# Kernel tuning notes

Measured on AMD Instinct MI355X. Metric: run time of the kernel, lower is better.

Reference implementation:

```python
import jax, jax.numpy as jnp
import numpy as np

N_NODES = 100000
N_EDGES = 1600000
D = 128
NEG_SLOPE = 0.01  # torch F.leaky_relu default


def setup_inputs() -> dict:
    key = jax.random.key(0)
    k1, k2, k3, k4, k5, k6 = jax.random.split(key, 6)
    input = jax.random.normal(k1, (N_NODES, D), dtype=jnp.float32)
    edge_row = jax.random.randint(k2, (N_EDGES,), 0, N_NODES, dtype=jnp.int32)
    edge_col = jax.random.randint(k3, (N_EDGES,), 0, N_NODES, dtype=jnp.int32)
    edge_val = jax.random.uniform(k4, (N_EDGES,), dtype=jnp.float32)
    # learned params: W1: Linear(D, D, bias=False), W2: Linear(2D, D, bias=False)
    # torch stores weight as [out, in]; apply as x @ W.T
    bound1 = 1.0 / np.sqrt(D)
    bound2 = 1.0 / np.sqrt(2 * D)
    W1 = jax.random.uniform(k5, (D, D), dtype=jnp.float32, minval=-bound1, maxval=bound1)
    W2 = jax.random.uniform(k6, (D, 2 * D), dtype=jnp.float32, minval=-bound2, maxval=bound2)
    return {"input": input, "edge_row": edge_row, "edge_col": edge_col,
            "edge_val": edge_val, "W1": W1, "W2": W2}


def reference(input, edge_row, edge_col, edge_val, W1, W2):
    # proj_input = W1(input)
    proj = input @ W1.T                                   # [N, D]
    # neighboor = spmm(adj, proj): out[i] = sum_e val[e] * proj[col[e]] for row[e]==i
    msg = edge_val[:, None] * proj[edge_col]              # [E, D]
    neigh = jax.ops.segment_sum(msg, edge_row, num_segments=input.shape[0])  # [N, D]
    h = jnp.concatenate([input + neigh, input * neigh], axis=-1)  # [N, 2D]
    return jax.nn.leaky_relu(h @ W2.T, NEG_SLOPE)         # [N, D]
```

## Files before the change

### kernel.cpp

```cpp
#include <hip/hip_runtime.h>

#define DIM 128
#define BROWS 128
#define BCAP 3072
#define NBUK_PAD 800
#define BK_EDGES 6144

typedef __attribute__((ext_vector_type(8))) short short8;
typedef __attribute__((ext_vector_type(4))) float f32x4;

__device__ __forceinline__ unsigned short f2bf(float f) {
    unsigned u = __float_as_uint(f);
    u += 0x7fffu + ((u >> 16) & 1u);
    return (unsigned short)(u >> 16);
}
__device__ __forceinline__ float bf2f(unsigned short b) {
    return __uint_as_float(((unsigned)b) << 16);
}

__global__ void k_zero(int* __restrict__ gcur, int nbuk) {
    int i = threadIdx.x;
    if (i < nbuk) gcur[i] = 0;
}

__global__ __launch_bounds__(1024) void k_prep(const float4* __restrict__ in,
                                               const float* __restrict__ W1,
                                               const float* __restrict__ W2,
                                               const int* __restrict__ er,
                                               const int* __restrict__ ec,
                                               const float* __restrict__ ev,
                                               int* __restrict__ gcur,
                                               int2* __restrict__ edata0,
                                               unsigned short* __restrict__ inputb,
                                               unsigned short* __restrict__ w1b,
                                               unsigned short* __restrict__ w2b,
                                               int E, int nbuk, int nBkt, int n4) {
    __shared__ int2 sed[BK_EDGES];
    __shared__ int lhist[NBUK_PAD];
    __shared__ int lscan[NBUK_PAD];
    __shared__ int lpos[NBUK_PAD];
    __shared__ int gbase[NBUK_PAD];
    int b = blockIdx.x, tid = threadIdx.x;

    if (b < nBkt) {
        if (tid < NBUK_PAD) lhist[tid] = 0;
        __syncthreads();
        int e0 = b * BK_EDGES;
        int bcnt = E - e0; if (bcnt > BK_EDGES) bcnt = BK_EDGES;
        for (int i = tid; i < bcnt; i += 1024)
            atomicAdd(&lhist[er[e0 + i] >> 7], 1);
        __syncthreads();
        if (tid < NBUK_PAD) lscan[tid] = lhist[tid];
        __syncthreads();
        for (int off = 1; off < NBUK_PAD; off <<= 1) {
            int v = (tid < NBUK_PAD && tid >= off) ? lscan[tid - off] : 0;
            __syncthreads();
            if (tid < NBUK_PAD) lscan[tid] += v;
            __syncthreads();
        }
        if (tid < NBUK_PAD) {
            int c = lhist[tid];
            lpos[tid] = lscan[tid] - c;
            gbase[tid] = (c > 0 && tid < nbuk) ? atomicAdd(&gcur[tid], c) : 0;
        }
        __syncthreads();
        for (int i = tid; i < bcnt; i += 1024) {
            int e = e0 + i;
            int r = er[e], bk = r >> 7;
            int p = atomicAdd(&lpos[bk], 1);
            sed[p] = make_int2(((r & 127) << 17) | ec[e], __float_as_int(ev[e]));
        }
        __syncthreads();
        int sub = tid & 7, bg = tid >> 3;
        for (int bk = bg; bk < nbuk; bk += 128) {
            int c = lhist[bk];
            if (c == 0) continue;
            int excl = lscan[bk] - c;
            int gb = gbase[bk];
            long base = (long)bk * BCAP;
            for (int j = sub; j < c; j += 8)
                if (gb + j < BCAP)
                    edata0[base + gb + j] = sed[excl + j];
        }
    } else if (b < nBkt + 48) {
        int idx = (b - nBkt) * 1024 + tid;
        if (idx < 16384)      w1b[idx] = f2bf(W1[idx]);
        else                  w2b[idx - 16384] = f2bf(W2[idx - 16384]);
    } else {
        int i = (b - nBkt - 48) * 1024 + tid;
        if (i < n4) {
            float4 v = in[i];
            *(ushort4*)(inputb + (long)i * 4) =
                make_ushort4(f2bf(v.x), f2bf(v.y), f2bf(v.z), f2bf(v.w));
        }
    }
}

__global__ __launch_bounds__(512) void k_gather(const unsigned short* __restrict__ xb,
                                                const int2* __restrict__ edata0,
                                                const int* __restrict__ gcur,
                                                unsigned short* __restrict__ aggb, int N) {
    __shared__ int2 sed[BCAP];
    __shared__ int hist[BROWS];
    __shared__ int hscan[BROWS];
    __shared__ int lcur[BROWS];
    int tid = threadIdx.x, b = blockIdx.x;
    int cnt = gcur[b]; if (cnt > BCAP) cnt = BCAP;
    const int2* e0 = edata0 + (long)b * BCAP;
    if (tid < BROWS) hist[tid] = 0;
    __syncthreads();
    for (int i = tid; i < cnt; i += 512) atomicAdd(&hist[e0[i].x >> 17], 1);
    __syncthreads();
    if (tid < BROWS) hscan[tid] = hist[tid];
    __syncthreads();
    for (int off = 1; off < BROWS; off <<= 1) {
        int v = (tid < BROWS && tid >= off) ? hscan[tid - off] : 0;
        __syncthreads();
        if (tid < BROWS) hscan[tid] += v;
        __syncthreads();
    }
    if (tid < BROWS) lcur[tid] = hscan[tid] - hist[tid];
    __syncthreads();
    for (int i = tid; i < cnt; i += 512) {
        int2 v = e0[i];
        int p = atomicAdd(&lcur[v.x >> 17], 1);
        sed[p] = make_int2(v.x & 0x1FFFF, v.y);
    }
    __syncthreads();

    int slot = tid >> 4, s = tid & 15;
    const int4* x4 = (const int4*)xb;

#define ACC8(U, V)                                                         \
    {                                                                      \
        const unsigned* wp_ = (const unsigned*)&(U);                       \
        pa[0] += (V) * __uint_as_float(wp_[0] << 16);                      \
        pa[1] += (V) * __uint_as_float(wp_[0] & 0xffff0000u);              \
        pa[2] += (V) * __uint_as_float(wp_[1] << 16);                      \
        pa[3] += (V) * __uint_as_float(wp_[1] & 0xffff0000u);              \
        pa[4] += (V) * __uint_as_float(wp_[2] << 16);                      \
        pa[5] += (V) * __uint_as_float(wp_[2] & 0xffff0000u);              \
        pa[6] += (V) * __uint_as_float(wp_[3] << 16);                      \
        pa[7] += (V) * __uint_as_float(wp_[3] & 0xffff0000u);              \
    }

    for (int k = 0; k < 4; ++k) {
        int rl = k * 32 + slot;
        int row = b * BROWS + rl;
        int beg = hscan[rl] - hist[rl], end = hscan[rl];
        float pa[8];
#pragma unroll
        for (int t = 0; t < 8; ++t) pa[t] = 0.f;
        int j = beg;
        for (; j + 4 <= end; j += 4) {
            int2 q0 = sed[j], q1 = sed[j + 1], q2 = sed[j + 2], q3 = sed[j + 3];
            int4 u0 = x4[(long)q0.x * 16 + s];
            int4 u1 = x4[(long)q1.x * 16 + s];
            int4 u2 = x4[(long)q2.x * 16 + s];
            int4 u3 = x4[(long)q3.x * 16 + s];
            float v0 = __int_as_float(q0.y), v1 = __int_as_float(q1.y);
            float v2 = __int_as_float(q2.y), v3 = __int_as_float(q3.y);
            ACC8(u0, v0);
            ACC8(u1, v1);
            ACC8(u2, v2);
            ACC8(u3, v3);
        }
        for (; j < end; ++j) {
            int2 q = sed[j];
            int4 u = x4[(long)q.x * 16 + s];
            float v = __int_as_float(q.y);
            ACC8(u, v);
        }
        if (row < N) {
            short8 o;
#pragma unroll
            for (int t = 0; t < 8; ++t) o[t] = (short)f2bf(pa[t]);
            *(short8*)(aggb + (long)row * DIM + s * 8) = o;
        }
    }
#undef ACC8
}

__global__ __launch_bounds__(256, 3) void k_fused(const unsigned short* __restrict__ aggb,
                                                  const unsigned short* __restrict__ inputb,
                                                  const unsigned short* __restrict__ w1b,
                                                  const unsigned short* __restrict__ w2b,
                                                  float* __restrict__ out, int N) {
    __shared__ __align__(16) unsigned short sh[2 * 64 * 136];
    __shared__ __align__(16) unsigned short xs[64 * 136];
    int w = threadIdx.x >> 6, lane = threadIdx.x & 63;
    int quad = lane >> 4, lq = lane & 15;
    int blk0 = blockIdx.x * 64;
    unsigned short* sh0 = sh;
    unsigned short* sh1 = sh + 64 * 136;

    for (int i = threadIdx.x; i < 64 * 16; i += 256) {
        int row = i >> 4, c = i & 15;
        int rr = blk0 + row; if (rr >= N) rr = N - 1;
        *(short8*)(xs + row * 136 + c * 8) =
            *(const short8*)(inputb + (long)rr * DIM + c * 8);
    }

    short8 b1[2][4];
#pragma unroll
    for (int ntl = 0; ntl < 2; ++ntl)
#pragma unroll
        for (int kb = 0; kb < 4; ++kb)
            b1[ntl][kb] = *(const short8*)(w1b + ((w * 2 + ntl) * 16 + lq) * DIM +
                                           kb * 32 + quad * 8);
    __syncthreads();

#pragma unroll
    for (int mt = 0; mt < 4; ++mt) {
        short8 afr[4];
        {
            int row = blk0 + mt * 16 + lq; if (row >= N) row = N - 1;
#pragma unroll
            for (int kb = 0; kb < 4; ++kb)
                afr[kb] = *(const short8*)(aggb + (long)row * DIM + kb * 32 + quad * 8);
        }
#pragma unroll
        for (int ntl = 0; ntl < 2; ++ntl) {
            f32x4 c = {0.f, 0.f, 0.f, 0.f};
#pragma unroll
            for (int kb = 0; kb < 4; ++kb)
                c = __builtin_amdgcn_mfma_f32_16x16x32_bf16(afr[kb], b1[ntl][kb], c, 0, 0, 0);
            int nt = w * 2 + ntl;
#pragma unroll
            for (int rg = 0; rg < 4; ++rg) {
                int lrow = mt * 16 + quad * 4 + rg;
                float x = bf2f(xs[lrow * 136 + nt * 16 + lq]);
                float nb = c[rg];
                int off = lrow * 136 + nt * 16 + lq;
                sh0[off] = f2bf(x + nb);
                sh1[off] = f2bf(x * nb);
            }
        }
    }

    short8 b2[2][8];
#pragma unroll
    for (int ntl = 0; ntl < 2; ++ntl)
#pragma unroll
        for (int kb = 0; kb < 8; ++kb)
            b2[ntl][kb] = *(const short8*)(w2b + ((w * 2 + ntl) * 16 + lq) * 256 +
                                           kb * 32 + quad * 8);
    __syncthreads();

#pragma unroll
    for (int mt = 0; mt < 4; ++mt) {
        int arow = (mt * 16 + lq) * 136;
        short8 a0[4], a1[4];
#pragma unroll
        for (int kb = 0; kb < 4; ++kb) {
            a0[kb] = *(const short8*)(sh0 + arow + kb * 32 + quad * 8);
            a1[kb] = *(const short8*)(sh1 + arow + kb * 32 + quad * 8);
        }
#pragma unroll
        for (int ntl = 0; ntl < 2; ++ntl) {
            f32x4 c = {0.f, 0.f, 0.f, 0.f};
#pragma unroll
            for (int kb = 0; kb < 4; ++kb)
                c = __builtin_amdgcn_mfma_f32_16x16x32_bf16(a0[kb], b2[ntl][kb], c, 0, 0, 0);
#pragma unroll
            for (int kb = 0; kb < 4; ++kb)
                c = __builtin_amdgcn_mfma_f32_16x16x32_bf16(a1[kb], b2[ntl][kb + 4], c, 0, 0, 0);
            int nt = w * 2 + ntl;
#pragma unroll
            for (int rg = 0; rg < 4; ++rg) {
                int r = blk0 + mt * 16 + quad * 4 + rg;
                if (r < N) {
                    float v = c[rg];
                    v = (v > 0.f) ? v : 0.01f * v;
                    out[(long)r * DIM + nt * 16 + lq] = v;
                }
            }
        }
    }
}

extern "C" void kernel_launch(void* const* d_in, const int* in_sizes, int n_in,
                              void* d_out, int out_size, void* d_ws, size_t ws_size,
                              hipStream_t stream) {
    const float* input = (const float*)d_in[0];
    const int*   er    = (const int*)d_in[1];
    const int*   ec    = (const int*)d_in[2];
    const float* ev    = (const float*)d_in[3];
    const float* W1    = (const float*)d_in[4];
    const float* W2    = (const float*)d_in[5];
    int N = in_sizes[0] / DIM;
    int E = in_sizes[1];
    float* out = (float*)d_out;
    int nbuk = (N + BROWS - 1) / BROWS;

    int* ws = (int*)d_ws;
    int* gcur = ws;
    int2* edata0 = (int2*)(ws + 1024);
    unsigned short* w1b = (unsigned short*)(edata0 + (long)nbuk * BCAP);
    unsigned short* w2b = w1b + 16384;
    unsigned short* inputb = w2b + 32768;
    unsigned short* aggb = inputb + (long)N * DIM;

    int n4 = N * (DIM / 4);
    int nBkt = (E + BK_EDGES - 1) / BK_EDGES;
    int nCvt = (n4 + 1023) / 1024;

    k_zero<<<1, 1024, 0, stream>>>(gcur, nbuk);

    k_prep<<<nBkt + 48 + nCvt, 1024, 0, stream>>>(
        (const float4*)input, W1, W2, er, ec, ev, gcur, edata0,
        inputb, w1b, w2b, E, nbuk, nBkt, n4);

    k_gather<<<nbuk, 512, 0, stream>>>(inputb, edata0, gcur, aggb, N);

    k_fused<<<(N + 63) / 64, 256, 0, stream>>>(aggb, inputb, w1b, w2b, out, N);
}
```

Before: 233.9 us.

## Halve fused GEMM shared tiles, unroll gather by 8, memset counters

The fused GEMM kernel now processes its 64 rows in two 32-row halves. This halves shared memory per block, loads W2 fragments per column tile instead of holding them all in registers, and raises the occupancy hint from 3 to 4 blocks. The gather inner loop gains an 8-edge unrolled stage so more independent global loads are in flight. The zeroing kernel is replaced by hipMemsetAsync. The trade-offs are an extra sync per half and W2 fragments being reloaded for each half.

```diff
diff --git a/kernel.cpp b/kernel.cpp
--- a/kernel.cpp
+++ b/kernel.cpp
@@ -16,11 +16,6 @@
 }
 __device__ __forceinline__ float bf2f(unsigned short b) {
     return __uint_as_float(((unsigned)b) << 16);
-}
-
-__global__ void k_zero(int* __restrict__ gcur, int nbuk) {
-    int i = threadIdx.x;
-    if (i < nbuk) gcur[i] = 0;
 }
 
 __global__ __launch_bounds__(1024) void k_prep(const float4* __restrict__ in,
@@ -152,24 +147,41 @@
 #pragma unroll
         for (int t = 0; t < 8; ++t) pa[t] = 0.f;
         int j = beg;
+        for (; j + 8 <= end; j += 8) {
+            int2 q0 = sed[j],     q1 = sed[j + 1], q2 = sed[j + 2], q3 = sed[j + 3];
+            int2 q4 = sed[j + 4], q5 = sed[j + 5], q6 = sed[j + 6], q7 = sed[j + 7];
+            int4 u0 = x4[(long)q0.x * 16 + s];
+            int4 u1 = x4[(long)q1.x * 16 + s];
+            int4 u2 = x4[(long)q2.x * 16 + s];
+            int4 u3 = x4[(long)q3.x * 16 + s];
+            int4 u4 = x4[(long)q4.x * 16 + s];
+            int4 u5 = x4[(long)q5.x * 16 + s];
+            int4 u6 = x4[(long)q6.x * 16 + s];
+            int4 u7 = x4[(long)q7.x * 16 + s];
+            ACC8(u0, __int_as_float(q0.y));
+            ACC8(u1, __int_as_float(q1.y));
+            ACC8(u2, __int_as_float(q2.y));
+            ACC8(u3, __int_as_float(q3.y));
+            ACC8(u4, __int_as_float(q4.y));
+            ACC8(u5, __int_as_float(q5.y));
+            ACC8(u6, __int_as_float(q6.y));
+            ACC8(u7, __int_as_float(q7.y));
+        }
         for (; j + 4 <= end; j += 4) {
             int2 q0 = sed[j], q1 = sed[j + 1], q2 = sed[j + 2], q3 = sed[j + 3];
             int4 u0 = x4[(long)q0.x * 16 + s];
             int4 u1 = x4[(long)q1.x * 16 + s];
             int4 u2 = x4[(long)q2.x * 16 + s];
             int4 u3 = x4[(long)q3.x * 16 + s];
-            float v0 = __int_as_float(q0.y), v1 = __int_as_float(q1.y);
-            float v2 = __int_as_float(q2.y), v3 = __int_as_float(q3.y);
-            ACC8(u0, v0);
-            ACC8(u1, v1);
-            ACC8(u2, v2);
-            ACC8(u3, v3);
+            ACC8(u0, __int_as_float(q0.y));
+            ACC8(u1, __int_as_float(q1.y));
+            ACC8(u2, __int_as_float(q2.y));
+            ACC8(u3, __int_as_float(q3.y));
         }
         for (; j < end; ++j) {
             int2 q = sed[j];
             int4 u = x4[(long)q.x * 16 + s];
-            float v = __int_as_float(q.y);
-            ACC8(u, v);
+            ACC8(u, __int_as_float(q.y));
         }
         if (row < N) {
             short8 o;
@@ -181,25 +193,18 @@
 #undef ACC8
 }
 
-__global__ __launch_bounds__(256, 3) void k_fused(const unsigned short* __restrict__ aggb,
+__global__ __launch_bounds__(256, 4) void k_fused(const unsigned short* __restrict__ aggb,
                                                   const unsigned short* __restrict__ inputb,
                                                   const unsigned short* __restrict__ w1b,
                                                   const unsigned short* __restrict__ w2b,
                                                   float* __restrict__ out, int N) {
-    __shared__ __align__(16) unsigned short sh[2 * 64 * 136];
-    __shared__ __align__(16) unsigned short xs[64 * 136];
+    __shared__ __align__(16) unsigned short sh[2 * 32 * 136];
+    __shared__ __align__(16) unsigned short xs[32 * 136];
     int w = threadIdx.x >> 6, lane = threadIdx.x & 63;
     int quad = lane >> 4, lq = lane & 15;
     int blk0 = blockIdx.x * 64;
     unsigned short* sh0 = sh;
-    unsigned short* sh1 = sh + 64 * 136;
-
-    for (int i = threadIdx.x; i < 64 * 16; i += 256) {
-        int row = i >> 4, c = i & 15;
-        int rr = blk0 + row; if (rr >= N) rr = N - 1;
-        *(short8*)(xs + row * 136 + c * 8) =
-            *(const short8*)(inputb + (long)rr * DIM + c * 8);
-    }
+    unsigned short* sh1 = sh + 32 * 136;
 
     short8 b1[2][4];
 #pragma unroll
@@ -208,71 +213,77 @@
         for (int kb = 0; kb < 4; ++kb)
             b1[ntl][kb] = *(const short8*)(w1b + ((w * 2 + ntl) * 16 + lq) * DIM +
                                            kb * 32 + quad * 8);
-    __syncthreads();
-
-#pragma unroll
-    for (int mt = 0; mt < 4; ++mt) {
-        short8 afr[4];
-        {
-            int row = blk0 + mt * 16 + lq; if (row >= N) row = N - 1;
-#pragma unroll
-            for (int kb = 0; kb < 4; ++kb)
-                afr[kb] = *(const short8*)(aggb + (long)row * DIM + kb * 32 + quad * 8);
-        }
+
+    for (int half = 0; half < 2; ++half) {
+        int base = blk0 + half * 32;
+
+        for (int i = threadIdx.x; i < 32 * 16; i += 256) {
+            int row = i >> 4, c = i & 15;
+            int rr = base + row; if (rr >= N) rr = N - 1;
+            *(short8*)(xs + row * 136 + c * 8) =
+                *(const short8*)(inputb + (long)rr * DIM + c * 8);
+        }
+        __syncthreads();
+
+#pragma unroll
+        for (int mt = 0; mt < 2; ++mt) {
+            short8 afr[4];
+            {
+                int row = base + mt * 16 + lq; if (row >= N) row = N - 1;
+#pragma unroll
+                for (int kb = 0; kb < 4; ++kb)
+                    afr[kb] = *(const short8*)(aggb + (long)row * DIM + kb * 32 + quad * 8);
+            }
+#pragma unroll
+            for (int ntl = 0; ntl < 2; ++ntl) {
+                f32x4 c = {0.f, 0.f, 0.f, 0.f};
+#pragma unroll
+                for (int kb = 0; kb < 4; ++kb)
+                    c = __builtin_amdgcn_mfma_f32_16x16x32_bf16(afr[kb], b1[ntl][kb], c, 0, 0, 0);
+                int nt = w * 2 + ntl;
+#pragma unroll
+                for (int rg = 0; rg < 4; ++rg) {
+                    int lrow = mt * 16 + quad * 4 + rg;
+                    float x = bf2f(xs[lrow * 136 + nt * 16 + lq]);
+                    float nb = c[rg];
+                    int off = lrow * 136 + nt * 16 + lq;
+                    sh0[off] = f2bf(x + nb);
+                    sh1[off] = f2bf(x * nb);
+                }
+            }
+        }
+        __syncthreads();
+
 #pragma unroll
         for (int ntl = 0; ntl < 2; ++ntl) {
-            f32x4 c = {0.f, 0.f, 0.f, 0.f};
-#pragma unroll
-            for (int kb = 0; kb < 4; ++kb)
-                c = __builtin_amdgcn_mfma_f32_16x16x32_bf16(afr[kb], b1[ntl][kb], c, 0, 0, 0);
+            short8 bb[8];
+#pragma unroll
+            for (int kb = 0; kb < 8; ++kb)
+                bb[kb] = *(const short8*)(w2b + ((w * 2 + ntl) * 16 + lq) * 256 +
+                                          kb * 32 + quad * 8);
             int nt = w * 2 + ntl;
 #pragma unroll
-            for (int rg = 0; rg < 4; ++rg) {
-                int lrow = mt * 16 + quad * 4 + rg;
-                float x = bf2f(xs[lrow * 136 + nt * 16 + lq]);
-                float nb = c[rg];
-                int off = lrow * 136 + nt * 16 + lq;
-                sh0[off] = f2bf(x + nb);
-                sh1[off] = f2bf(x * nb);
-            }
-        }
-    }
-
-    short8 b2[2][8];
-#pragma unroll
-    for (int ntl = 0; ntl < 2; ++ntl)
-#pragma unroll
-        for (int kb = 0; kb < 8; ++kb)
-            b2[ntl][kb] = *(const short8*)(w2b + ((w * 2 + ntl) * 16 + lq) * 256 +
-                                           kb * 32 + quad * 8);
-    __syncthreads();
-
-#pragma unroll
-    for (int mt = 0; mt < 4; ++mt) {
-        int arow = (mt * 16 + lq) * 136;
-        short8 a0[4], a1[4];
-#pragma unroll
-        for (int kb = 0; kb < 4; ++kb) {
-            a0[kb] = *(const short8*)(sh0 + arow + kb * 32 + quad * 8);
-            a1[kb] = *(const short8*)(sh1 + arow + kb * 32 + quad * 8);
-        }
-#pragma unroll
-        for (int ntl = 0; ntl < 2; ++ntl) {
-            f32x4 c = {0.f, 0.f, 0.f, 0.f};
-#pragma unroll
-            for (int kb = 0; kb < 4; ++kb)
-                c = __builtin_amdgcn_mfma_f32_16x16x32_bf16(a0[kb], b2[ntl][kb], c, 0, 0, 0);
-#pragma unroll
-            for (int kb = 0; kb < 4; ++kb)
-                c = __builtin_amdgcn_mfma_f32_16x16x32_bf16(a1[kb], b2[ntl][kb + 4], c, 0, 0, 0);
-            int nt = w * 2 + ntl;
-#pragma unroll
-            for (int rg = 0; rg < 4; ++rg) {
-                int r = blk0 + mt * 16 + quad * 4 + rg;
-                if (r < N) {
-                    float v = c[rg];
-                    v = (v > 0.f) ? v : 0.01f * v;
-                    out[(long)r * DIM + nt * 16 + lq] = v;
+            for (int mt = 0; mt < 2; ++mt) {
+                int arow = (mt * 16 + lq) * 136;
+                f32x4 c = {0.f, 0.f, 0.f, 0.f};
+#pragma unroll
+                for (int kb = 0; kb < 4; ++kb) {
+                    short8 a0 = *(const short8*)(sh0 + arow + kb * 32 + quad * 8);
+                    c = __builtin_amdgcn_mfma_f32_16x16x32_bf16(a0, bb[kb], c, 0, 0, 0);
+                }
+#pragma unroll
+                for (int kb = 0; kb < 4; ++kb) {
+                    short8 a1 = *(const short8*)(sh1 + arow + kb * 32 + quad * 8);
+                    c = __builtin_amdgcn_mfma_f32_16x16x32_bf16(a1, bb[kb + 4], c, 0, 0, 0);
+                }
+#pragma unroll
+                for (int rg = 0; rg < 4; ++rg) {
+                    int r = base + mt * 16 + quad * 4 + rg;
+                    if (r < N) {
+                        float v = c[rg];
+                        v = (v > 0.f) ? v : 0.01f * v;
+                        out[(long)r * DIM + nt * 16 + lq] = v;
+                    }
                 }
             }
         }
@@ -305,7 +316,7 @@
     int nBkt = (E + BK_EDGES - 1) / BK_EDGES;
     int nCvt = (n4 + 1023) / 1024;
 
-    k_zero<<<1, 1024, 0, stream>>>(gcur, nbuk);
+    hipMemsetAsync(gcur, 0, (size_t)nbuk * sizeof(int), stream);
 
     k_prep<<<nBkt + 48 + nCvt, 1024, 0, stream>>>(
         (const float4*)input, W1, W2, er, ec, ev, gcur, edata0,
```

New measurement: 258.9 us. +10.7%, slower.
